# Kernel tuning notes

Hardware: AMD Instinct MI355X
Metric: run time of the kernel (lower is better)

## Reference

```python
import jax, jax.numpy as jnp
import numpy as np
from jax import lax

NUM_CLASSES = 5
K_MAX = 5
PROTO_DIM = 32
MARGIN = 1.0
ANCHOR_STRENGTH = 1.0
LAMBDA_COMPACT = 0.1
MAX_ANCHORS = 2048
KMEANS_ITERS = 5
EPS = 1e-12


def _normalize(x, axis=-1):
    return x / jnp.sqrt(jnp.sum(x * x, axis=axis, keepdims=True) + EPS)


def _cdist(a, b):
    # Euclidean distance matrix (n, m) via the squared-norm expansion.
    d2 = (jnp.sum(a * a, 1)[:, None] + jnp.sum(b * b, 1)[None, :] - 2.0 * (a @ b.T))
    return jnp.sqrt(jnp.maximum(d2, 0.0))


def _class_centroids(feats, mask, key):
    # feats: (N, D) L2-normalized; mask: (N,) bool selecting this class's voxels.
    N, D = feats.shape
    w = mask.astype(feats.dtype)
    cnt = w.sum()
    mean = (feats * w[:, None]).sum(0) / jnp.maximum(cnt, 1.0)

    def kmeans(_):
        k_init, k_fb = jax.random.split(key)
        # random init: K distinct masked points (gumbel top-k == randperm sample)
        g0 = jax.random.gumbel(k_init, (N,))
        _, init_idx = lax.top_k(jnp.where(mask, g0, -jnp.inf), K_MAX)
        cent0 = feats[init_idx]
        # fallback random masked points for empty clusters, one set per iter
        g2 = jax.random.gumbel(k_fb, (KMEANS_ITERS, N))
        fb_idx = jax.vmap(lambda s: lax.top_k(jnp.where(mask, s, -jnp.inf), K_MAX)[1])(g2)

        def body(cent, fb):
            d = _cdist(feats, cent)                       # (N, K)
            assign = jnp.argmin(d, axis=1)
            onehot = ((assign[:, None] == jnp.arange(K_MAX)[None, :]) & mask[:, None]).astype(feats.dtype)
            counts = onehot.sum(0)                        # (K,)
            sums = onehot.T @ feats                       # (K, D)
            newc = sums / jnp.maximum(counts, 1.0)[:, None]
            newc = jnp.where(counts[:, None] > 0, newc, feats[fb])
            return newc, None

        cent, _ = lax.scan(body, cent0, fb_idx)
        return _normalize(cent)

    def mean_rep(_):
        return jnp.tile(mean[None, :], (K_MAX, 1))

    cent = lax.cond(cnt >= K_MAX, kmeans, mean_rep, None)
    return _normalize(cent), cnt


def _loss_triplet(feats, prototypes, pseudo_masks, gt_masks, labeled_batch):
    B, Df, Zf, Yf, Xf = feats.shape
    N = B * Zf * Yf * Xf
    feats_flat = _normalize(jnp.transpose(feats, (0, 2, 3, 4, 1)).reshape(N, Df))
    # masks are already at feature resolution -> nearest interp is identity
    gt_flat = gt_masks.reshape(-1)
    pseudo_flat = pseudo_masks.reshape(-1)
    protos = _normalize(prototypes)                       # (C, K, D)
    key = jax.random.key(42)

    # ---- anchor loss: match prototypes to per-class kmeans centroids ----
    anchor_loss = jnp.float32(0.0)
    anchor_cnt = jnp.float32(0.0)
    for i in range(int(labeled_batch.shape[0])):
        c = labeled_batch[i]
        c_safe = jnp.clip(c, 0, NUM_CLASSES - 1)
        cmask = gt_flat == c
        cent, cnt = _class_centroids(feats_flat, cmask, jax.random.fold_in(key, i))
        valid = ((c != 0) & (c < NUM_CLASSES) & (cnt > 0)).astype(jnp.float32)
        loss_c = jnp.mean((protos[c_safe] - cent) ** 2)
        anchor_loss = anchor_loss + valid * loss_c
        anchor_cnt = anchor_cnt + valid
    anchor_loss = anchor_loss / jnp.maximum(anchor_cnt, 1.0)

    # ---- compactness: unbiased variance across the K prototypes per class ----
    compact_loss = jnp.var(protos[1:], axis=1, ddof=1).mean(axis=1).sum()

    # ---- triplet loss over pseudo-labeled anchors ----
    amask = pseudo_flat > 0
    ga = jax.random.gumbel(jax.random.fold_in(key, 1000), (N,))
    top_s, aidx = lax.top_k(jnp.where(amask, ga, -jnp.inf), MAX_ANCHORS)
    sel_valid = jnp.isfinite(top_s)                        # padding if < MAX_ANCHORS anchors
    a_feats = feats_flat[aidx]                             # (A, D)
    a_labels = jnp.clip(pseudo_flat[aidx], 0, NUM_CLASSES - 1)

    CK = NUM_CLASSES * K_MAX
    protos_flat = protos.reshape(CK, Df)
    col_cls = jnp.arange(CK) // K_MAX
    own = col_cls[None, :] == a_labels[:, None]            # (A, CK)

    sim = a_feats @ protos_flat.T
    pos_idx = jnp.argmax(jnp.where(own, sim, -jnp.inf), axis=1)
    pos_vecs = protos_flat[pos_idx]

    d_all = _cdist(a_feats, protos_flat)                   # (A, CK)
    pos_d = jnp.min(jnp.where(own, d_all, jnp.inf), axis=1)
    neg = ~own
    semi = neg & (d_all > pos_d[:, None]) & (d_all < pos_d[:, None] + MARGIN)
    g1 = jax.random.gumbel(jax.random.fold_in(key, 2000), (MAX_ANCHORS, CK))
    g2 = jax.random.gumbel(jax.random.fold_in(key, 2001), (MAX_ANCHORS, CK))
    idx_semi = jnp.argmax(jnp.where(semi, g1, -jnp.inf), axis=1)
    idx_rand = jnp.argmax(jnp.where(neg, g2, -jnp.inf), axis=1)
    neg_idx = jnp.where(semi.any(axis=1), idx_semi, idx_rand)
    neg_vecs = protos_flat[neg_idx]

    aN, pN, nN = _normalize(a_feats), _normalize(pos_vecs), _normalize(neg_vecs)
    d_pos = jnp.sqrt(jnp.sum((aN - pN) ** 2, axis=1) + EPS)
    d_neg = jnp.sqrt(jnp.sum((aN - nN) ** 2, axis=1) + EPS)
    wA = (sel_valid & (a_labels != 0)).astype(jnp.float32)
    proto_loss = jnp.sum(jax.nn.softplus(d_pos - d_neg + MARGIN) * wA) / jnp.maximum(wA.sum(), 1.0)

    return proto_loss + ANCHOR_STRENGTH * anchor_loss + LAMBDA_COMPACT * compact_loss


def setup_inputs() -> dict:
    key = jax.random.key(0)
    k1, k2, k3, k4 = jax.random.split(key, 4)
    B, Z = 4, 64
    feats = jax.random.normal(k1, (B, PROTO_DIM, Z, Z, Z), dtype=jnp.float32)
    protos = jax.random.normal(k2, (NUM_CLASSES, K_MAX, PROTO_DIM), dtype=jnp.float32)
    protos = _normalize(protos)
    pseudo_masks = jax.random.randint(k3, (B, Z, Z, Z), 0, NUM_CLASSES, dtype=jnp.int32)
    gt_masks = jax.random.randint(k4, (B, Z, Z, Z), 0, NUM_CLASSES, dtype=jnp.int32)
    labeled_batch = jnp.array([1, 2, 3, 4], dtype=jnp.int32)
    return {"feats": feats, "prototypes": protos, "pseudo_masks": pseudo_masks,
            "gt_masks": gt_masks, "labeled_batch": labeled_batch}


def reference(feats, prototypes, pseudo_masks, gt_masks, labeled_batch):
    return _loss_triplet(feats, prototypes, pseudo_masks, gt_masks, labeled_batch)
```

## Files before the change

### kernel.cpp

```cpp
#include <hip/hip_runtime.h>
#include <stdint.h>

typedef unsigned int u32;
typedef unsigned long long u64;

#define NCLS 5
#define KMX 5
#define DD 32
#define LBN 4
#define KIT 5
#define MAXA 2048
#define CKK 25
#define NBLKA 256
#define SCPAD 36
#define PSTRIDE 680
#define ACAP 8192
#define UKTHR ((1u << 23) + 1u - (1u << 15))
#define FTINY 1.17549435e-38f

struct RKeys {
  u32 ki[LBN][2];
  u32 kf[LBN][2];
  u32 k1000[2];
  u32 k2000[2];
  u32 k2001[2];
};

struct SelState {
  u32 prefix1, rank1, prefix21, rank2, pivot_sv, target, M, ncand, ncand2;
};

__host__ __device__ inline void tf2x32(u32 k0, u32 k1, u32 x0, u32 x1, u32* o0, u32* o1) {
  u32 ks2 = k0 ^ k1 ^ 0x1BD11BDAu;
  u32 ks[3] = {k0, k1, ks2};
  x0 += k0; x1 += k1;
  const int rotA[4] = {13, 15, 26, 6};
  const int rotB[4] = {17, 29, 16, 24};
#pragma unroll
  for (int g = 0; g < 5; ++g) {
#pragma unroll
    for (int j = 0; j < 4; ++j) {
      int r = (g & 1) ? rotB[j] : rotA[j];
      x0 += x1;
      x1 = (x1 << r) | (x1 >> (32 - r));
      x1 ^= x0;
    }
    x0 += ks[(g + 1) % 3];
    x1 += ks[(g + 2) % 3] + (u32)(g + 1);
  }
  *o0 = x0; *o1 = x1;
}

__device__ inline u32 jax_ukey(u32 k0, u32 k1, u32 half, u32 idx) {
  bool hi = (idx >= half);
  u32 c0 = hi ? (idx - half) : idx;
  u32 c1 = hi ? idx : (idx + half);
  u32 o0, o1;
  tf2x32(k0, k1, c0, c1, &o0, &o1);
  u32 bits = hi ? o1 : o0;
  return (bits >> 9) + 1u;
}

#define INS5(kk, a0, a1, a2, a3, a4) do { u64 _k = (kk); \
  if (_k > a4) { a4 = _k; u64 _t; \
    if (a4 > a3) { _t = a3; a3 = a4; a4 = _t; } \
    if (a3 > a2) { _t = a2; a2 = a3; a3 = _t; } \
    if (a2 > a1) { _t = a1; a1 = a2; a2 = _t; } \
    if (a1 > a0) { _t = a0; a0 = a1; a1 = _t; } } } while (0)

#define WMERGE5(off, a0, a1, a2, a3, a4) do { \
  u64 r0 = __shfl_xor(a0, off, 64), r1 = __shfl_xor(a1, off, 64), \
      r2 = __shfl_xor(a2, off, 64), r3 = __shfl_xor(a3, off, 64), \
      r4 = __shfl_xor(a4, off, 64); \
  INS5(r0, a0, a1, a2, a3, a4); INS5(r1, a0, a1, a2, a3, a4); \
  INS5(r2, a0, a1, a2, a3, a4); INS5(r3, a0, a1, a2, a3, a4); \
  INS5(r4, a0, a1, a2, a3, a4); } while (0)

#define WMERGE_ALL(a0,a1,a2,a3,a4) do { \
  WMERGE5(32,a0,a1,a2,a3,a4); WMERGE5(16,a0,a1,a2,a3,a4); WMERGE5(8,a0,a1,a2,a3,a4); \
  WMERGE5(4,a0,a1,a2,a3,a4); WMERGE5(2,a0,a1,a2,a3,a4); WMERGE5(1,a0,a1,a2,a3,a4); } while (0)

__device__ inline float rsum32(float v) {
#pragma unroll
  for (int o = 16; o; o >>= 1) v += __shfl_xor(v, o, 32);
  return v;
}

__device__ inline float rsum64(float v) {
#pragma unroll
  for (int o = 32; o; o >>= 1) v += __shfl_xor(v, o, 64);
  return v;
}


__global__ void k_protos(const float* __restrict__ protos, float* __restrict__ protn, float* __restrict__ compact) {
  __shared__ float pl[CKK * DD];
  __shared__ float rn[CKK];
  __shared__ float red[4];
  int tid = threadIdx.x;
  for (int t = tid; t < CKK * DD; t += 256) pl[t] = protos[t];
  __syncthreads();
  if (tid < CKK) {
    float s = 0.f;
    for (int d = 0; d < DD; ++d) { float x = pl[tid * DD + d]; s += x * x; }
    rn[tid] = sqrtf(s + 1e-12f);
  }
  __syncthreads();
  for (int t = tid; t < CKK * DD; t += 256) {
    float v = pl[t] / rn[t / DD];
    pl[t] = v;
    protn[t] = v;
  }
  __syncthreads();
  float part = 0.f;
  if (tid < (NCLS - 1) * DD) {
    int c = 1 + tid / DD;
    int d = tid % DD;
    float m = 0.f;
#pragma unroll
    for (int k = 0; k < KMX; ++k) m += pl[(c * KMX + k) * DD + d];
    m *= (1.0f / KMX);
    float v = 0.f;
#pragma unroll
    for (int k = 0; k < KMX; ++k) { float df = pl[(c * KMX + k) * DD + d] - m; v += df * df; }
    part = v * (1.0f / (KMX - 1)) * (1.0f / DD);
  }
#pragma unroll
  for (int o = 32; o; o >>= 1) part += __shfl_xor(part, o, 64);
  int wid = tid >> 6;
  if ((tid & 63) == 0) red[wid] = part;
  __syncthreads();
  if (tid == 0) compact[0] = red[0] + red[1] + red[2] + red[3];
}


#define T5PROC_THR(gv_, nn_) do { \
  int ci = (gv_ == lb0) ? 0 : (gv_ == lb1) ? 1 : (gv_ == lb2) ? 2 : (gv_ == lb3) ? 3 : -1; \
  if (ci >= 0) { \
    u32 k0 = (ci & 2) ? ((ci & 1) ? ka3 : ka2) : ((ci & 1) ? ka1 : ka0); \
    u32 k1 = (ci & 2) ? ((ci & 1) ? kb3 : kb2) : ((ci & 1) ? kb1 : kb0); \
    u32 uk = jax_ukey(k0, k1, half, base + (u32)(nn_)); \
    if (uk >= UKTHR) { \
      u64 key = ((u64)uk << 32) | (u32)(~(u32)(nn_)); \
      if (ci == 0) { INS5(key, A0, A1, A2, A3, A4); } \
      else if (ci == 1) { INS5(key, B0, B1, B2, B3, B4); } \
      else if (ci == 2) { INS5(key, C0, C1, C2, C3, C4); } \
      else { INS5(key, D0, D1, D2, D3, D4); } \
    } \
  } } while (0)

#define T5PROC(gv_, nn_) do { \
  int ci = (gv_ == lb0) ? 0 : (gv_ == lb1) ? 1 : (gv_ == lb2) ? 2 : (gv_ == lb3) ? 3 : -1; \
  if (ci >= 0) { \
    u32 k0 = (ci & 2) ? ((ci & 1) ? ka3 : ka2) : ((ci & 1) ? ka1 : ka0); \
    u32 k1 = (ci & 2) ? ((ci & 1) ? kb3 : kb2) : ((ci & 1) ? kb1 : kb0); \
    u32 uk = jax_ukey(k0, k1, half, base + (u32)(nn_)); \
    u64 key = ((u64)uk << 32) | (u32)(~(u32)(nn_)); \
    if (ci == 0) { INS5(key, A0, A1, A2, A3, A4); } \
    else if (ci == 1) { INS5(key, B0, B1, B2, B3, B4); } \
    else if (ci == 2) { INS5(key, C0, C1, C2, C3, C4); } \
    else { INS5(key, D0, D1, D2, D3, D4); } \
  } } while (0)

#define T5_TAIL_STORE() \
  WMERGE_ALL(A0,A1,A2,A3,A4); \
  WMERGE_ALL(B0,B1,B2,B3,B4); \
  WMERGE_ALL(C0,C1,C2,C3,C4); \
  WMERGE_ALL(D0,D1,D2,D3,D4); \
  __shared__ u64 wbuf[4][20]; \
  int tid = threadIdx.x; \
  int wid = tid >> 6; \
  if ((tid & 63) == 0) { \
    u64* w = wbuf[wid]; \
    w[0]=A0; w[1]=A1; w[2]=A2; w[3]=A3; w[4]=A4; \
    w[5]=B0; w[6]=B1; w[7]=B2; w[8]=B3; w[9]=B4; \
    w[10]=C0; w[11]=C1; w[12]=C2; w[13]=C3; w[14]=C4; \
    w[15]=D0; w[16]=D1; w[17]=D2; w[18]=D3; w[19]=D4; \
  } \
  __syncthreads(); \
  if (tid == 0) { \
    _Pragma("unroll") \
    for (int w = 1; w < 4; ++w) { \
      _Pragma("unroll") \
      for (int j = 0; j < 5; ++j) { \
        u64 ka = wbuf[w][j];      INS5(ka, A0, A1, A2, A3, A4); \
        u64 kb = wbuf[w][5 + j];  INS5(kb, B0, B1, B2, B3, B4); \
        u64 kc = wbuf[w][10 + j]; INS5(kc, C0, C1, C2, C3, C4); \
        u64 kd = wbuf[w][15 + j]; INS5(kd, D0, D1, D2, D3, D4); \
      } \
    } \
    size_t nb = gridDim.x; \
    u64* o0 = outA + (((size_t)kind * LBN + 0) * nb + blockIdx.x) * 5; \
    o0[0]=A0; o0[1]=A1; o0[2]=A2; o0[3]=A3; o0[4]=A4; \
    u64* o1 = outA + (((size_t)kind * LBN + 1) * nb + blockIdx.x) * 5; \
    o1[0]=B0; o1[1]=B1; o1[2]=B2; o1[3]=B3; o1[4]=B4; \
    u64* o2 = outA + (((size_t)kind * LBN + 2) * nb + blockIdx.x) * 5; \
    o2[0]=C0; o2[1]=C1; o2[2]=C2; o2[3]=C3; o2[4]=C4; \
    u64* o3 = outA + (((size_t)kind * LBN + 3) * nb + blockIdx.x) * 5; \
    o3[0]=D0; o3[1]=D1; o3[2]=D2; o3[3]=D3; o3[4]=D4; \
  }

#define T5_HEAD() \
  int kind = blockIdx.y; \
  int lb0 = labeled[0], lb1 = labeled[1], lb2 = labeled[2], lb3 = labeled[3]; \
  u32 half = (kind == 0) ? (u32)(N / 2) : (u32)(((u64)5 * (u64)N) / 2); \
  u32 base = (kind == 0) ? 0u : (u32)((u64)(kind - 1) * (u64)N); \
  u32 ka0 = (kind == 0) ? RK.ki[0][0] : RK.kf[0][0], kb0 = (kind == 0) ? RK.ki[0][1] : RK.kf[0][1]; \
  u32 ka1 = (kind == 0) ? RK.ki[1][0] : RK.kf[1][0], kb1 = (kind == 0) ? RK.ki[1][1] : RK.kf[1][1]; \
  u32 ka2 = (kind == 0) ? RK.ki[2][0] : RK.kf[2][0], kb2 = (kind == 0) ? RK.ki[2][1] : RK.kf[2][1]; \
  u32 ka3 = (kind == 0) ? RK.ki[3][0] : RK.kf[3][0], kb3 = (kind == 0) ? RK.ki[3][1] : RK.kf[3][1]; \
  u64 A0=0,A1=0,A2=0,A3=0,A4=0; \
  u64 B0=0,B1=0,B2=0,B3=0,B4=0; \
  u64 C0=0,C1=0,C2=0,C3=0,C4=0; \
  u64 D0=0,D1=0,D2=0,D3=0,D4=0;

__global__ void k_top5A(const int* __restrict__ gt, const int* __restrict__ labeled,
                        RKeys RK, u64* __restrict__ outA, int N) {
  T5_HEAD()
  int Nq = N >> 2;
  int stride = gridDim.x * blockDim.x;
  for (int q = blockIdx.x * blockDim.x + threadIdx.x; q < Nq; q += stride) {
    int4 g4 = ((const int4*)gt)[q];
    int n = q << 2;
    T5PROC_THR(g4.x, n);
    T5PROC_THR(g4.y, n + 1);
    T5PROC_THR(g4.z, n + 2);
    T5PROC_THR(g4.w, n + 3);
  }
  T5_TAIL_STORE()
}

__global__ void k_top5B(const u64* __restrict__ outA, u32* __restrict__ rescue,
                        u64* __restrict__ top5F, int nblk) {
  int kind = blockIdx.x;
  int i = blockIdx.y;
  const u64* src = outA + ((size_t)kind * LBN + i) * nblk * 5;
  u64 t0 = 0, t1 = 0, t2 = 0, t3 = 0, t4 = 0;
  int tot = nblk * 5;
  for (int j = threadIdx.x; j < tot; j += blockDim.x) { u64 k = src[j]; INS5(k, t0, t1, t2, t3, t4); }
  WMERGE_ALL(t0, t1, t2, t3, t4);
  __shared__ u64 wbuf[4 * 5];
  int tid = threadIdx.x;
  int wid = tid >> 6;
  if ((tid & 63) == 0) {
    wbuf[wid * 5 + 0] = t0; wbuf[wid * 5 + 1] = t1; wbuf[wid * 5 + 2] = t2;
    wbuf[wid * 5 + 3] = t3; wbuf[wid * 5 + 4] = t4;
  }
  __syncthreads();
  if (tid == 0) {
#pragma unroll
    for (int w = 1; w < 4; ++w)
#pragma unroll
      for (int j = 0; j < 5; ++j) { u64 k = wbuf[w * 5 + j]; INS5(k, t0, t1, t2, t3, t4); }
    u64* o = top5F + ((size_t)kind * LBN + i) * 5;
    o[0] = t0; o[1] = t1; o[2] = t2; o[3] = t3; o[4] = t4;
    if (t4 == 0ULL) atomicOr(rescue, 1u << (kind * 4 + i));
  }
}

__global__ void k_top5A_resc(const int* __restrict__ gt, const int* __restrict__ labeled,
                             RKeys RK, const u32* __restrict__ rescue,
                             u64* __restrict__ outA, int N) {
  if (((rescue[0] >> (blockIdx.y * 4)) & 0xFu) == 0u) return;
  T5_HEAD()
  int Nq = N >> 2;
  int stride = gridDim.x * blockDim.x;
  for (int q = blockIdx.x * blockDim.x + threadIdx.x; q < Nq; q += stride) {
    int4 g4 = ((const int4*)gt)[q];
    int n = q << 2;
    T5PROC(g4.x, n);
    T5PROC(g4.y, n + 1);
    T5PROC(g4.z, n + 2);
    T5PROC(g4.w, n + 3);
  }
  T5_TAIL_STORE()
}

__global__ void k_top5B_resc(const u64* __restrict__ outA, const u32* __restrict__ rescue,
                             u64* __restrict__ top5F, int nblk) {
  int kind = blockIdx.x;
  int i = blockIdx.y;
  if (!((rescue[0] >> (kind * 4 + i)) & 1u)) return;
  const u64* src = outA + ((size_t)kind * LBN + i) * nblk * 5;
  u64 t0 = 0, t1 = 0, t2 = 0, t3 = 0, t4 = 0;
  int tot = nblk * 5;
  for (int j = threadIdx.x; j < tot; j += blockDim.x) { u64 k = src[j]; INS5(k, t0, t1, t2, t3, t4); }
  WMERGE_ALL(t0, t1, t2, t3, t4);
  __shared__ u64 wbuf[4 * 5];
  int tid = threadIdx.x;
  int wid = tid >> 6;
  if ((tid & 63) == 0) {
    wbuf[wid * 5 + 0] = t0; wbuf[wid * 5 + 1] = t1; wbuf[wid * 5 + 2] = t2;
    wbuf[wid * 5 + 3] = t3; wbuf[wid * 5 + 4] = t4;
  }
  __syncthreads();
  if (tid == 0) {
#pragma unroll
    for (int w = 1; w < 4; ++w)
#pragma unroll
      for (int j = 0; j < 5; ++j) { u64 k = wbuf[w * 5 + j]; INS5(k, t0, t1, t2, t3, t4); }
    u64* o = top5F + ((size_t)kind * LBN + i) * 5;
    o[0] = t0; o[1] = t1; o[2] = t2; o[3] = t3; o[4] = t4;
  }
}


__global__ void __launch_bounds__(256)
k_normT(const float* __restrict__ feats, float4* __restrict__ featsN4, int N, int Z3) {
  __shared__ float xl[256 * 33];
  __shared__ float sinv[256];
  int tid = threadIdx.x;
  int nchunk = N >> 8;
  for (int chunk = blockIdx.x; chunk < nchunk; chunk += gridDim.x) {
    int n0 = chunk << 8;
    int b = n0 / Z3, v0 = n0 - b * Z3;
    const float* fp = feats + (size_t)b * DD * Z3 + v0 + tid;
#pragma unroll
    for (int d = 0; d < DD; ++d) xl[tid * 33 + d] = fp[(size_t)d * Z3];
    float s = 0.f;
#pragma unroll
    for (int d = 0; d < DD; ++d) { float x = xl[tid * 33 + d]; s += x * x; }
    sinv[tid] = 1.0f / sqrtf(s + 1e-12f);
    __syncthreads();
#pragma unroll
    for (int i = 0; i < 8; ++i) {
      int fi = i * 256 + tid;
      int vox = fi >> 3, q = fi & 7;
      float iv = sinv[vox];
      float4 o;
      o.x = xl[vox * 33 + q * 4 + 0] * iv;
      o.y = xl[vox * 33 + q * 4 + 1] * iv;
      o.z = xl[vox * 33 + q * 4 + 2] * iv;
      o.w = xl[vox * 33 + q * 4 + 3] * iv;
      featsN4[(size_t)n0 * 8 + fi] = o;
    }
    __syncthreads();
  }
}

__global__ void k_initcentT(const float* __restrict__ featsN,
                            const u64* __restrict__ top5F, float* __restrict__ cent, int N) {
  int t = threadIdx.x;
  if (t >= LBN * KMX * DD) return;
  int d = t & 31;
  int k = (t >> 5) % KMX;
  int i = t / (KMX * DD);
  u32 n = ~(u32)(top5F[((size_t)0 * LBN + i) * 5 + k]);
  if (n >= (u32)N) n = 0;
  cent[(i * KMX + k) * DD + d] = featsN[(size_t)n * DD + d];
}

__global__ void __launch_bounds__(256)
k_assignW2(const float4* __restrict__ featsN4, const int* __restrict__ gt,
           const int* __restrict__ labeled, const float* __restrict__ cent,
           float* __restrict__ part, int N) {
  __shared__ float sc[LBN * KMX * SCPAD];
  __shared__ float ssw[8][LBN * KMX * SCPAD];
  __shared__ float scn[LBN * KMX];
  __shared__ float scw[8][LBN * KMX];
  int tid = threadIdx.x;
  for (int t = tid; t < LBN * KMX * DD; t += 256) {
    int cl2 = t >> 5, d = t & 31;
    sc[cl2 * SCPAD + d] = cent[t];
  }
  for (int t = tid; t < 8 * LBN * KMX * SCPAD; t += 256) (&ssw[0][0])[t] = 0.f;
  for (int t = tid; t < 8 * LBN * KMX; t += 256) (&scw[0][0])[t] = 0.f;
  __syncthreads();
  if (tid < LBN * KMX) {
    float s = 0.f;
#pragma unroll
    for (int d = 0; d < DD; ++d) { float c = sc[tid * SCPAD + d]; s += c * c; }
    scn[tid] = s;
  }
  __syncthreads();
  int lb0 = labeled[0], lb1 = labeled[1], lb2 = labeled[2], lb3 = labeled[3];
  int q = tid & 7;
  int grp = (tid >> 3) & 7;
  int wv = tid >> 6;
  int cpi = 2 * wv + (grp >> 2);
  float* myss = &ssw[cpi][0];
  float* mysc = &scw[cpi][0];
  int sstep = grp & 3;
  const float* scq = sc + q * 4;
  int nchunk = N >> 5;
  int chunk = blockIdx.x;
  if (chunk < nchunk) {
    float4 f4 = featsN4[(size_t)chunk * 256 + tid];
    int g = gt[(chunk << 5) + (tid >> 3)];
    while (true) {
      int nxt = chunk + gridDim.x;
      bool has = nxt < nchunk;
      float4 nf4; int ng = 0;
      if (has) {
        nf4 = featsN4[(size_t)nxt * 256 + tid];
        ng = gt[(nxt << 5) + (tid >> 3)];
      }
      int ci = (g == lb0) ? 0 : (g == lb1) ? 1 : (g == lb2) ? 2 : (g == lb3) ? 3 : -1;
      int basec = (ci < 0 ? 0 : ci) * KMX;
      float4 c0 = *(const float4*)(scq + (basec + 0) * SCPAD);
      float4 c1 = *(const float4*)(scq + (basec + 1) * SCPAD);
      float4 c2 = *(const float4*)(scq + (basec + 2) * SCPAD);
      float4 c3 = *(const float4*)(scq + (basec + 3) * SCPAD);
      float4 c4 = *(const float4*)(scq + (basec + 4) * SCPAD);
      float p0 = f4.x * c0.x + f4.y * c0.y + f4.z * c0.z + f4.w * c0.w;
      float p1 = f4.x * c1.x + f4.y * c1.y + f4.z * c1.z + f4.w * c1.w;
      float p2 = f4.x * c2.x + f4.y * c2.y + f4.z * c2.z + f4.w * c2.w;
      float p3 = f4.x * c3.x + f4.y * c3.y + f4.z * c3.z + f4.w * c3.w;
      float p4 = f4.x * c4.x + f4.y * c4.y + f4.z * c4.z + f4.w * c4.w;
#pragma unroll
      for (int o = 1; o < 8; o <<= 1) {
        p0 += __shfl_xor(p0, o, 64);
        p1 += __shfl_xor(p1, o, 64);
        p2 += __shfl_xor(p2, o, 64);
        p3 += __shfl_xor(p3, o, 64);
        p4 += __shfl_xor(p4, o, 64);
      }
      float bd = scn[basec + 0] - 2.0f * p0; int bk = 0;
      float d2;
      d2 = scn[basec + 1] - 2.0f * p1; if (d2 < bd) { bd = d2; bk = 1; }
      d2 = scn[basec + 2] - 2.0f * p2; if (d2 < bd) { bd = d2; bk = 2; }
      d2 = scn[basec + 3] - 2.0f * p3; if (d2 < bd) { bd = d2; bk = 3; }
      d2 = scn[basec + 4] - 2.0f * p4; if (d2 < bd) { bd = d2; bk = 4; }
      int cl = basec + bk;
#pragma unroll
      for (int s = 0; s < 4; ++s) {
        if (sstep == s && ci >= 0) {
          float* dst = myss + cl * SCPAD + q * 4;
          float4 cur = *(float4*)dst;
          cur.x += f4.x; cur.y += f4.y; cur.z += f4.z; cur.w += f4.w;
          *(float4*)dst = cur;
          if (q == 0) mysc[cl] += 1.0f;
        }
      }
      if (!has) break;
      chunk = nxt; f4 = nf4; g = ng;
    }
  }
  __syncthreads();
  float* po = part + (size_t)blockIdx.x * PSTRIDE;
  for (int p = tid; p < 660; p += 256) {
    float v;
    if (p < 640) {
      int idx = (p >> 5) * SCPAD + (p & 31);
      v = ssw[0][idx] + ssw[1][idx] + ssw[2][idx] + ssw[3][idx]
        + ssw[4][idx] + ssw[5][idx] + ssw[6][idx] + ssw[7][idx];
    } else {
      int ik = p - 640;
      v = scw[0][ik] + scw[1][ik] + scw[2][ik] + scw[3][ik]
        + scw[4][ik] + scw[5][ik] + scw[6][ik] + scw[7][ik];
    }
    po[p] = v;
  }
}

__global__ void k_redupdT(const float* __restrict__ part, const float* __restrict__ featsN,
                          const u64* __restrict__ top5F, float* __restrict__ cent,
                          float* __restrict__ sums, float* __restrict__ kcnt,
                          int iter, int N, int NB) {
  __shared__ float w4[8];
  int p = blockIdx.x;
  int tid = threadIdx.x;
  if (p < 640) {
    int ik = p >> 5, d = p & 31;
    float s = 0.f, c = 0.f;
    for (int b2 = tid; b2 < NB; b2 += 256) {
      s += part[(size_t)b2 * PSTRIDE + p];
      c += part[(size_t)b2 * PSTRIDE + 640 + ik];
    }
    s = rsum64(s); c = rsum64(c);
    int wid = tid >> 6;
    if ((tid & 63) == 0) { w4[wid] = s; w4[4 + wid] = c; }
    __syncthreads();
    if (tid == 0) {
      float S = w4[0] + w4[1] + w4[2] + w4[3];
      float C = w4[4] + w4[5] + w4[6] + w4[7];
      sums[p] = S;
      if (C > 0.f) {
        cent[p] = S / fmaxf(C, 1.0f);
      } else {
        int i = ik / KMX, k = ik % KMX;
        u32 n = ~(u32)(top5F[((size_t)(1 + iter) * LBN + i) * 5 + k]);
        if (n >= (u32)N) n = 0;
        cent[p] = featsN[(size_t)n * DD + d];
      }
    }
  } else if (p < 660) {
    int ik = p - 640;
    float c = 0.f;
    for (int b2 = tid; b2 < NB; b2 += 256) c += part[(size_t)b2 * PSTRIDE + 640 + ik];
    c = rsum64(c);
    int wid = tid >> 6;
    if ((tid & 63) == 0) w4[wid] = c;
    __syncthreads();
    if (tid == 0) kcnt[ik] = w4[0] + w4[1] + w4[2] + w4[3];
  }
}

__global__ void k_prepT(const float4* __restrict__ featsN4,
                        const int* __restrict__ pseudo, const SelState* __restrict__ st,
                        const int* __restrict__ aidx, float4* __restrict__ afe4,
                        int* __restrict__ alab, int N) {
  int tid = threadIdx.x;
  int r = blockIdx.x * 32 + (tid >> 3);
  int q = tid & 7;
  if (r >= (int)st->target) return;
  int n = aidx[r];
  if ((u32)n >= (u32)N) n = 0;
  if (q == 0) {
    int lb = pseudo[n];
    alab[r] = lb < 0 ? 0 : (lb > NCLS - 1 ? NCLS - 1 : lb);
  }
  afe4[(size_t)r * 8 + q] = featsN4[(size_t)n * 8 + q];
}


__global__ void __launch_bounds__(256)
k_anchsel(const int* __restrict__ pseudo, RKeys RK, u64* __restrict__ cand8k,
          SelState* st, int N) {
  __shared__ u32 mcnt[4];
  u32 K0 = RK.k1000[0], K1 = RK.k1000[1];
  u32 half = (u32)(N / 2);
  int tid = threadIdx.x;
  int lcnt = 0;
  int stride = gridDim.x * blockDim.x;
  for (int n = blockIdx.x * blockDim.x + tid; n < N; n += stride) {
    bool valid = pseudo[n] > 0;
    lcnt += valid ? 1 : 0;
    u32 uk = jax_ukey(K0, K1, half, (u32)n);
    bool c = valid && (uk >= UKTHR);
    if (__ballot(c)) {
      if (c) {
        u32 p = atomicAdd(&st->ncand, 1u);
        if (p < (u32)ACAP) cand8k[p] = ((u64)uk << 32) | (u32)(~(u32)n);
      }
    }
  }
#pragma unroll
  for (int o = 32; o; o >>= 1) lcnt += __shfl_xor(lcnt, o, 64);
  if ((tid & 63) == 0) mcnt[tid >> 6] = (u32)lcnt;
  __syncthreads();
  if (tid == 0) atomicAdd(&st->M, mcnt[0] + mcnt[1] + mcnt[2] + mcnt[3]);
}

__global__ void k_selmode(SelState* st, u32* rescue) {
  if (threadIdx.x != 0 || blockIdx.x != 0) return;
  u32 M = st->M;
  u32 tgt = M < (u32)MAXA ? M : (u32)MAXA;
  st->target = tgt;
  if (!(st->ncand >= tgt && st->ncand <= (u32)ACAP)) rescue[1] = 1u;
}

__global__ void __launch_bounds__(1024)
k_sortsel8k(const u64* __restrict__ cand8k, const SelState* __restrict__ st,
            const u32* __restrict__ rescue, int* __restrict__ aidx) {
  if (rescue[1]) return;
  __shared__ u64 s[ACAP];
  u32 nc = st->ncand; if (nc > (u32)ACAP) nc = (u32)ACAP;
  u32 target = st->target;
  for (int t = threadIdx.x; t < ACAP; t += blockDim.x) s[t] = (t < (int)nc) ? cand8k[t] : 0ULL;
  __syncthreads();
  for (u32 ksz = 2; ksz <= (u32)ACAP; ksz <<= 1) {
    for (u32 j = ksz >> 1; j > 0; j >>= 1) {
      for (u32 idx = threadIdx.x; idx < (u32)ACAP; idx += blockDim.x) {
        u32 ixj = idx ^ j;
        if (ixj > idx) {
          bool up = (idx & ksz) == 0;
          u64 A = s[idx], B = s[ixj];
          bool sw = up ? (A < B) : (A > B);
          if (sw) { s[idx] = B; s[ixj] = A; }
        }
      }
      __syncthreads();
    }
  }
  for (int t = threadIdx.x; t < MAXA; t += blockDim.x)
    if (t < (int)target) aidx[t] = (int)(~(u32)s[t]);
}


__global__ void k_svinit(const int* __restrict__ pseudo, RKeys RK, const u32* __restrict__ rescue,
                         u32* __restrict__ sv, u32* __restrict__ hist, int N) {
  if (!rescue[1]) return;
  __shared__ u32 h[2048];
  for (int t = threadIdx.x; t < 2048; t += blockDim.x) h[t] = 0;
  __syncthreads();
  u32 half = (u32)(N / 2);
  u32 K0 = RK.k1000[0], K1 = RK.k1000[1];
  int Nq = N >> 2;
  int stride = gridDim.x * blockDim.x;
  for (int q = blockIdx.x * blockDim.x + threadIdx.x; q < Nq; q += stride) {
    int4 p4 = ((const int4*)pseudo)[q];
    int n = q << 2;
    u32 s0 = 0, s1 = 0, s2 = 0, s3 = 0;
    if (p4.x > 0) { s0 = jax_ukey(K0, K1, half, (u32)n);     atomicAdd(&h[s0 >> 21], 1u); }
    if (p4.y > 0) { s1 = jax_ukey(K0, K1, half, (u32)n + 1); atomicAdd(&h[s1 >> 21], 1u); }
    if (p4.z > 0) { s2 = jax_ukey(K0, K1, half, (u32)n + 2); atomicAdd(&h[s2 >> 21], 1u); }
    if (p4.w > 0) { s3 = jax_ukey(K0, K1, half, (u32)n + 3); atomicAdd(&h[s3 >> 21], 1u); }
    ((uint4*)sv)[q] = make_uint4(s0, s1, s2, s3);
  }
  __syncthreads();
  for (int t = threadIdx.x; t < 2048; t += blockDim.x) if (h[t]) atomicAdd(&hist[t], h[t]);
}

__global__ void k_hist12(const u32* __restrict__ sv, u32* __restrict__ hist,
                         const SelState* __restrict__ st, const u32* __restrict__ rescue,
                         int pass, int N) {
  if (!rescue[1]) return;
  __shared__ u32 h[2048];
  for (int t = threadIdx.x; t < 2048; t += blockDim.x) h[t] = 0;
  __syncthreads();
  u32 pre = (pass == 1) ? st->prefix1 : st->prefix21;
  int Nq = N >> 2;
  int stride = gridDim.x * blockDim.x;
  for (int q = blockIdx.x * blockDim.x + threadIdx.x; q < Nq; q += stride) {
    uint4 s4 = ((const uint4*)sv)[q];
#define H12(s_) do { u32 s = (s_); if (s) { \
      if (pass == 1) { if ((s >> 21) == pre) atomicAdd(&h[(s >> 10) & 0x7FFu], 1u); } \
      else           { if ((s >> 10) == pre) atomicAdd(&h[s & 0x3FFu], 1u); } } } while (0)
    H12(s4.x); H12(s4.y); H12(s4.z); H12(s4.w);
#undef H12
  }
  __syncthreads();
  for (int t = threadIdx.x; t < 2048; t += blockDim.x) if (h[t]) atomicAdd(&hist[t], h[t]);
}

__global__ void k_scan(const u32* __restrict__ hist, SelState* st,
                       const u32* __restrict__ rescue, int pass) {
  if (!rescue[1]) return;
  __shared__ u32 h[2048];
  __shared__ u32 csum[256];
  __shared__ u32 sh_rank;
  __shared__ int sh_found;
  __shared__ u32 sh_rem;
  int tid = threadIdx.x;
  int nb = (pass == 2) ? 1024 : 2048;
  for (int t = tid; t < 2048; t += 256) h[t] = (t < nb) ? hist[t] : 0u;
  __syncthreads();
  u32 cs = 0;
#pragma unroll
  for (int j = 0; j < 8; ++j) cs += h[tid * 8 + j];
  csum[tid] = cs;
  __syncthreads();
  if (tid == 0) {
    sh_rank = (pass == 0) ? st->target : (pass == 1 ? st->rank1 : st->rank2);
    sh_found = -1;
    sh_rem = 0;
  }
  __syncthreads();
  u32 rank = sh_rank;
  if (rank > 0) {
    u32 above = 0;
    for (int j = tid + 1; j < 256; ++j) above += csum[j];
    u32 run = above;
    for (int b = tid * 8 + 7; b >= tid * 8; --b) {
      u32 c = h[b];
      if (run < rank && rank <= run + c) { sh_found = b; sh_rem = rank - run; }
      run += c;
    }
  }
  __syncthreads();
  if (tid == 0) {
    int found = sh_found;
    u32 rem = sh_rem;
    if (pass == 0) {
      if (found < 0) { st->prefix1 = 0xFFFFFFFFu; st->rank1 = 0; }
      else { st->prefix1 = (u32)found; st->rank1 = rem; }
    } else if (pass == 1) {
      if (found < 0) { st->prefix21 = 0xFFFFFFFFu; st->rank2 = 0; }
      else { st->prefix21 = (st->prefix1 << 11) | (u32)found; st->rank2 = rem; }
    } else {
      if (found < 0) st->pivot_sv = 0xFFFFFFFFu;
      else st->pivot_sv = (st->prefix21 << 10) | (u32)found;
    }
  }
}

__global__ void k_gather(const u32* __restrict__ sv, SelState* st,
                         const u32* __restrict__ rescue, u64* __restrict__ cand, int N) {
  if (!rescue[1]) return;
  if (st->target == 0) return;
  u32 piv = st->pivot_sv;
  int Nq = N >> 2;
  int stride = gridDim.x * blockDim.x;
  for (int q = blockIdx.x * blockDim.x + threadIdx.x; q < Nq; q += stride) {
    uint4 s4 = ((const uint4*)sv)[q];
    int n = q << 2;
#define GPUSH(s_, nn_) do { u32 s = (s_); \
    if (s && s >= piv) { u32 p = atomicAdd(&st->ncand2, 1u); \
      if (p < 4096u) cand[p] = ((u64)s << 32) | (u32)(~(u32)(nn_)); } } while (0)
    GPUSH(s4.x, n); GPUSH(s4.y, n + 1); GPUSH(s4.z, n + 2); GPUSH(s4.w, n + 3);
#undef GPUSH
  }
}

__global__ void __launch_bounds__(1024) k_sortsel(const u64* __restrict__ cand,
                                                  const SelState* __restrict__ st,
                                                  const u32* __restrict__ rescue,
                                                  int* __restrict__ aidx) {
  if (!rescue[1]) return;
  __shared__ u64 s[4096];
  u32 nc = st->ncand2; if (nc > 4096u) nc = 4096u;
  u32 target = st->target;
  for (int t = threadIdx.x; t < 4096; t += blockDim.x) s[t] = (t < (int)nc) ? cand[t] : 0ULL;
  __syncthreads();
  for (u32 ksz = 2; ksz <= 4096; ksz <<= 1) {
    for (u32 j = ksz >> 1; j > 0; j >>= 1) {
      for (u32 idx = threadIdx.x; idx < 4096; idx += blockDim.x) {
        u32 ixj = idx ^ j;
        if (ixj > idx) {
          bool up = (idx & ksz) == 0;
          u64 A = s[idx], B = s[ixj];
          bool sw = up ? (A < B) : (A > B);
          if (sw) { s[idx] = B; s[ixj] = A; }
        }
      }
      __syncthreads();
    }
  }
  for (int t = threadIdx.x; t < MAXA; t += blockDim.x)
    if (t < (int)target) aidx[t] = (int)(~(u32)s[t]);
}


__global__ void k_anchor_final(const float* __restrict__ cent, const float* __restrict__ sums,
                               const float* __restrict__ kcnt, const float* __restrict__ protn,
                               const int* __restrict__ labeled, float* __restrict__ accum) {
  int i = blockIdx.x;
  int d = threadIdx.x;
  if (d >= DD) return;
  int c = labeled[i];
  float cnt = 0.f;
#pragma unroll
  for (int k = 0; k < KMX; ++k) cnt += kcnt[i * KMX + k];
  int cs = c < 0 ? 0 : (c > NCLS - 1 ? NCLS - 1 : c);
  float part = 0.f;
  if (cnt >= (float)KMX) {
#pragma unroll
    for (int k = 0; k < KMX; ++k) {
      float v = cent[(i * KMX + k) * DD + d];
      float s = rsum32(v * v);
      float dn1 = sqrtf(s + 1e-12f);
      float v1 = v / dn1;
      float s2 = rsum32(v1 * v1);
      float dn2 = sqrtf(s2 + 1e-12f);
      float vv = v1 / dn2;
      float df = protn[(cs * KMX + k) * DD + d] - vv;
      part += df * df;
    }
  } else {
    float mv = 0.f;
#pragma unroll
    for (int k = 0; k < KMX; ++k) mv += sums[(i * KMX + k) * DD + d];
    mv /= fmaxf(cnt, 1.0f);
    float s = rsum32(mv * mv);
    float dn = sqrtf(s + 1e-12f);
    float vv = mv / dn;
#pragma unroll
    for (int k = 0; k < KMX; ++k) {
      float df = protn[(cs * KMX + k) * DD + d] - vv;
      part += df * df;
    }
  }
  float ls = rsum32(part) * (1.0f / (KMX * DD));
  bool valid = (c != 0) && (c < NCLS) && (cnt > 0.f);
  if (d == 0 && valid) { atomicAdd(&accum[0], ls); atomicAdd(&accum[1], 1.0f); }
}

__global__ void k_triplet(const float* __restrict__ protn, const float* __restrict__ afe,
                          const int* __restrict__ alab, const SelState* __restrict__ st,
                          RKeys RK, float* __restrict__ acc) {
  __shared__ float pn[CKK * DD];
  __shared__ float spn[CKK];
  int tid = threadIdx.x;
  for (int t = tid; t < CKK * DD; t += blockDim.x) pn[t] = protn[t];
  __syncthreads();
  if (tid < CKK) {
    float s = 0.f;
    for (int d = 0; d < DD; ++d) s += pn[tid * DD + d] * pn[tid * DD + d];
    spn[tid] = s;
  }
  __syncthreads();
  int r = blockIdx.x * blockDim.x + tid;
  if (r >= (int)st->target) return;
  float a[DD]; float sa = 0.f;
#pragma unroll
  for (int d = 0; d < DD; ++d) { a[d] = afe[(size_t)r * DD + d]; sa += a[d] * a[d]; }
  int lab = alab[r];
  int ob = lab * KMX;
  float bs = -3.4e38f; int pidx = ob;
  float pos_d = 3.4e38f;
  for (int k = ob; k < ob + KMX; ++k) {
    float dot = 0.f;
#pragma unroll
    for (int d = 0; d < DD; ++d) dot += a[d] * pn[k * DD + d];
    if (dot > bs) { bs = dot; pidx = k; }
    float d2 = (sa + spn[k]) - 2.0f * dot;
    float dd = sqrtf(fmaxf(d2, 0.f));
    pos_d = fminf(pos_d, dd);
  }
  u32 halfT = (u32)(MAXA * CKK / 2);
  bool any_semi = false;
  u32 bu1 = 0; int k1i = 0;
  u32 bu2 = 0; int k2i = 0;
  for (int k = 0; k < CKK; ++k) {
    if (k / KMX == lab) continue;
    float dot = 0.f;
#pragma unroll
    for (int d = 0; d < DD; ++d) dot += a[d] * pn[k * DD + d];
    float d2 = (sa + spn[k]) - 2.0f * dot;
    float dd = sqrtf(fmaxf(d2, 0.f));
    u32 j = (u32)(r * CKK + k);
    bool semi = (dd > pos_d) && (dd < pos_d + 1.0f);
    if (semi) {
      u32 u1 = jax_ukey(RK.k2000[0], RK.k2000[1], halfT, j);
      any_semi = true;
      if (u1 > bu1) { bu1 = u1; k1i = k; }
    }
    u32 u2 = jax_ukey(RK.k2001[0], RK.k2001[1], halfT, j);
    if (u2 > bu2) { bu2 = u2; k2i = k; }
  }
  int nidx = any_semi ? k1i : k2i;
  float aden = sqrtf(sa + 1e-12f);
  float pden = sqrtf(spn[pidx] + 1e-12f);
  float nden = sqrtf(spn[nidx] + 1e-12f);
  float s1 = 0.f, s2 = 0.f;
#pragma unroll
  for (int d = 0; d < DD; ++d) {
    float an = a[d] / aden;
    float pv = pn[pidx * DD + d] / pden;
    float nv = pn[nidx * DD + d] / nden;
    float t1 = an - pv; s1 += t1 * t1;
    float t2 = an - nv; s2 += t2 * t2;
  }
  float d_pos = sqrtf(s1 + 1e-12f);
  float d_neg = sqrtf(s2 + 1e-12f);
  float xx = (d_pos - d_neg) + 1.0f;
  float l = fmaxf(xx, 0.f) + log1pf(expf(-fabsf(xx)));
  atomicAdd(&acc[0], l);
  atomicAdd(&acc[1], 1.0f);
}

__global__ void k_final(const float* __restrict__ anchor_acc, const float* __restrict__ proto_acc,
                        const float* __restrict__ compact, float* __restrict__ out) {
  if (threadIdx.x != 0 || blockIdx.x != 0) return;
  float al = anchor_acc[0] / fmaxf(anchor_acc[1], 1.0f);
  float pl = proto_acc[0] / fmaxf(proto_acc[1], 1.0f);
  out[0] = pl + 1.0f * al + 0.1f * compact[0];
}


static void host_keys(RKeys* K) {
  const u32 b0 = 0u, b1 = 42u;
  u32 o0, o1;
  for (int i = 0; i < LBN; ++i) {
    u32 f0, f1;
    tf2x32(b0, b1, 0u, (u32)i, &f0, &f1);
    u32 p0, q0, p1, q1;
    tf2x32(f0, f1, 0u, 2u, &p0, &q0);
    tf2x32(f0, f1, 1u, 3u, &p1, &q1);
    K->ki[i][0] = p0; K->ki[i][1] = p1;
    K->kf[i][0] = q0; K->kf[i][1] = q1;
  }
  tf2x32(b0, b1, 0u, 1000u, &o0, &o1); K->k1000[0] = o0; K->k1000[1] = o1;
  tf2x32(b0, b1, 0u, 2000u, &o0, &o1); K->k2000[0] = o0; K->k2000[1] = o1;
  tf2x32(b0, b1, 0u, 2001u, &o0, &o1); K->k2001[0] = o0; K->k2001[1] = o1;
}

extern "C" void kernel_launch(void* const* d_in, const int* in_sizes, int n_in,
                              void* d_out, int out_size, void* d_ws, size_t ws_size,
                              hipStream_t stream) {
  const float* feats = (const float*)d_in[0];
  const float* protos = (const float*)d_in[1];
  const int* pseudo = (const int*)d_in[2];
  const int* gt = (const int*)d_in[3];
  const int* labeled = (const int*)d_in[4];
  float* out = (float*)d_out;

  int N = in_sizes[2];
  int Z3 = N / 4;

  RKeys RK;
  host_keys(&RK);

  const int nbas[3] = {1280, 640, 320};
  for (int attempt = 0; attempt < 3; ++attempt) {
    int NBAS = nbas[attempt];
    char* W = (char*)d_ws;
    size_t off = 0;
    auto alloc = [&](size_t bytes) -> char* {
      char* p = W + off;
      off += (bytes + 255) & ~(size_t)255;
      return p;
    };
    char* zeroBase = W + off;
    u32* hist3 = (u32*)alloc(3 * 2048 * 4);
    SelState* st = (SelState*)alloc(256);
    float* anchor_acc = (float*)alloc(256);
    float* proto_acc = (float*)alloc(256);
    u32* rescue = (u32*)alloc(256);
    size_t zeroBytes = (size_t)((W + off) - zeroBase);
    u64* cand8k = (u64*)alloc((size_t)ACAP * 8);
    u64* outA = (u64*)alloc((size_t)6 * LBN * NBLKA * 5 * 8);
    u64* top5F = (u64*)alloc((size_t)6 * LBN * 5 * 8);
    float* cent = (float*)alloc((size_t)LBN * KMX * DD * 4);
    float* sums = (float*)alloc((size_t)LBN * KMX * DD * 4);
    float* kcnt = (float*)alloc((size_t)LBN * KMX * 4);
    float* protn = (float*)alloc((size_t)CKK * DD * 4);
    float* compact = (float*)alloc(256);
    u32* sv = (u32*)alloc((size_t)N * 4);
    float* part = (float*)alloc((size_t)NBAS * PSTRIDE * 4);
    u64* cand = (u64*)alloc(4096 * 8);
    int* aidx = (int*)alloc((size_t)MAXA * 4);
    int* alab = (int*)alloc((size_t)MAXA * 4);
    float* afe = (float*)alloc((size_t)MAXA * DD * 4);
    float* featsN = (float*)alloc((size_t)N * DD * 4);
    if (ws_size < off) continue;

    hipMemsetAsync(zeroBase, 0, zeroBytes, stream);

    k_protos<<<dim3(1), dim3(256), 0, stream>>>(protos, protn, compact);

    k_top5A<<<dim3(NBLKA, 6), dim3(256), 0, stream>>>(gt, labeled, RK, outA, N);
    k_top5B<<<dim3(6, LBN), dim3(256), 0, stream>>>(outA, rescue, top5F, NBLKA);
    k_top5A_resc<<<dim3(NBLKA, 6), dim3(256), 0, stream>>>(gt, labeled, RK, rescue, outA, N);
    k_top5B_resc<<<dim3(6, LBN), dim3(256), 0, stream>>>(outA, rescue, top5F, NBLKA);

    float4* featsN4 = (float4*)featsN;
    k_normT<<<dim3(2048), dim3(256), 0, stream>>>(feats, featsN4, N, Z3);
    k_initcentT<<<dim3(1), dim3(LBN * KMX * DD), 0, stream>>>(featsN, top5F, cent, N);
    for (int it = 0; it < KIT; ++it) {
      k_assignW2<<<dim3(NBAS), dim3(256), 0, stream>>>(featsN4, gt, labeled, cent, part, N);
      k_redupdT<<<dim3(660), dim3(256), 0, stream>>>(part, featsN, top5F, cent, sums, kcnt, it, N, NBAS);
    }
    k_anchor_final<<<dim3(LBN), dim3(64), 0, stream>>>(cent, sums, kcnt, protn, labeled, anchor_acc);

    k_anchsel<<<dim3(2048), dim3(256), 0, stream>>>(pseudo, RK, cand8k, st, N);
    k_selmode<<<dim3(1), dim3(64), 0, stream>>>(st, rescue);
    k_svinit<<<dim3(1024), dim3(256), 0, stream>>>(pseudo, RK, rescue, sv, hist3, N);
    k_scan<<<dim3(1), dim3(256), 0, stream>>>(hist3, st, rescue, 0);
    k_hist12<<<dim3(1024), dim3(256), 0, stream>>>(sv, hist3 + 2048, st, rescue, 1, N);
    k_scan<<<dim3(1), dim3(256), 0, stream>>>(hist3 + 2048, st, rescue, 1);
    k_hist12<<<dim3(1024), dim3(256), 0, stream>>>(sv, hist3 + 4096, st, rescue, 2, N);
    k_scan<<<dim3(1), dim3(256), 0, stream>>>(hist3 + 4096, st, rescue, 2);
    k_gather<<<dim3(1024), dim3(256), 0, stream>>>(sv, st, rescue, cand, N);
    k_sortsel<<<dim3(1), dim3(1024), 0, stream>>>(cand, st, rescue, aidx);
    k_sortsel8k<<<dim3(1), dim3(1024), 0, stream>>>(cand8k, st, rescue, aidx);

    k_prepT<<<dim3(MAXA / 32), dim3(256), 0, stream>>>(featsN4, pseudo, st, aidx,
                                                        (float4*)afe, alab, N);
    k_triplet<<<dim3(MAXA / 256), dim3(256), 0, stream>>>(protn, afe, alab, st, RK, proto_acc);

    k_final<<<dim3(1), dim3(64), 0, stream>>>(anchor_acc, proto_acc, compact, out);
    return;
  }
}
```

Measured before the change: 681.1 us.

## Replace single-block bitonic sort with multi-block rank-by-counting selection

The single-workgroup 8192-element bitonic sort of anchor candidates is replaced by a rank computation spread across 16 blocks: each thread counts how many candidate keys exceed its own and writes its index to that rank slot if it falls under the target. The candidate capacity is halved to 4096, which shrinks shared memory and the O(n^2) counting work. The cost is that fewer candidate sets fit in the fast path, so more inputs may fall back to the slower histogram-based rescue path. Each block also reloads every key into LDS.

Result: faster. 614.3 us (-9.8%).

```diff
diff --git a/kernel.cpp b/kernel.cpp
--- a/kernel.cpp
+++ b/kernel.cpp
@@ -14,7 +14,7 @@
 #define NBLKA 256
 #define SCPAD 36
 #define PSTRIDE 680
-#define ACAP 8192
+#define ACAP 4096
 #define UKTHR ((1u << 23) + 1u - (1u << 15))
 #define FTINY 1.17549435e-38f
 
@@ -515,7 +515,7 @@
 
 
 __global__ void __launch_bounds__(256)
-k_anchsel(const int* __restrict__ pseudo, RKeys RK, u64* __restrict__ cand8k,
+k_anchsel(const int* __restrict__ pseudo, RKeys RK, u64* __restrict__ cand4k,
           SelState* st, int N) {
   __shared__ u32 mcnt[4];
   u32 K0 = RK.k1000[0], K1 = RK.k1000[1];
@@ -531,7 +531,7 @@
     if (__ballot(c)) {
       if (c) {
         u32 p = atomicAdd(&st->ncand, 1u);
-        if (p < (u32)ACAP) cand8k[p] = ((u64)uk << 32) | (u32)(~(u32)n);
+        if (p < (u32)ACAP) cand4k[p] = ((u64)uk << 32) | (u32)(~(u32)n);
       }
     }
   }
@@ -550,31 +550,22 @@
   if (!(st->ncand >= tgt && st->ncand <= (u32)ACAP)) rescue[1] = 1u;
 }
 
-__global__ void __launch_bounds__(1024)
-k_sortsel8k(const u64* __restrict__ cand8k, const SelState* __restrict__ st,
-            const u32* __restrict__ rescue, int* __restrict__ aidx) {
+__global__ void __launch_bounds__(256)
+k_rank(const u64* __restrict__ cand4k, const SelState* __restrict__ st,
+       const u32* __restrict__ rescue, int* __restrict__ aidx) {
   if (rescue[1]) return;
-  __shared__ u64 s[ACAP];
+  __shared__ u64 keys[ACAP];
   u32 nc = st->ncand; if (nc > (u32)ACAP) nc = (u32)ACAP;
   u32 target = st->target;
-  for (int t = threadIdx.x; t < ACAP; t += blockDim.x) s[t] = (t < (int)nc) ? cand8k[t] : 0ULL;
-  __syncthreads();
-  for (u32 ksz = 2; ksz <= (u32)ACAP; ksz <<= 1) {
-    for (u32 j = ksz >> 1; j > 0; j >>= 1) {
-      for (u32 idx = threadIdx.x; idx < (u32)ACAP; idx += blockDim.x) {
-        u32 ixj = idx ^ j;
-        if (ixj > idx) {
-          bool up = (idx & ksz) == 0;
-          u64 A = s[idx], B = s[ixj];
-          bool sw = up ? (A < B) : (A > B);
-          if (sw) { s[idx] = B; s[ixj] = A; }
-        }
-      }
-      __syncthreads();
-    }
-  }
-  for (int t = threadIdx.x; t < MAXA; t += blockDim.x)
-    if (t < (int)target) aidx[t] = (int)(~(u32)s[t]);
+  int tid = threadIdx.x;
+  for (int t = tid; t < ACAP; t += 256) keys[t] = (t < (int)nc) ? cand4k[t] : 0ULL;
+  __syncthreads();
+  int i = blockIdx.x * 256 + tid;
+  if (i >= (int)nc) return;
+  u64 my = keys[i];
+  u32 rank = 0;
+  for (u32 j = 0; j < nc; ++j) rank += (keys[j] > my) ? 1u : 0u;
+  if (rank < target) aidx[rank] = (int)(~(u32)my);
 }
 
 
@@ -899,7 +890,7 @@
     float* proto_acc = (float*)alloc(256);
     u32* rescue = (u32*)alloc(256);
     size_t zeroBytes = (size_t)((W + off) - zeroBase);
-    u64* cand8k = (u64*)alloc((size_t)ACAP * 8);
+    u64* cand4k = (u64*)alloc((size_t)ACAP * 8);
     u64* outA = (u64*)alloc((size_t)6 * LBN * NBLKA * 5 * 8);
     u64* top5F = (u64*)alloc((size_t)6 * LBN * 5 * 8);
     float* cent = (float*)alloc((size_t)LBN * KMX * DD * 4);
@@ -934,7 +925,7 @@
     }
     k_anchor_final<<<dim3(LBN), dim3(64), 0, stream>>>(cent, sums, kcnt, protn, labeled, anchor_acc);
 
-    k_anchsel<<<dim3(2048), dim3(256), 0, stream>>>(pseudo, RK, cand8k, st, N);
+    k_anchsel<<<dim3(2048), dim3(256), 0, stream>>>(pseudo, RK, cand4k, st, N);
     k_selmode<<<dim3(1), dim3(64), 0, stream>>>(st, rescue);
     k_svinit<<<dim3(1024), dim3(256), 0, stream>>>(pseudo, RK, rescue, sv, hist3, N);
     k_scan<<<dim3(1), dim3(256), 0, stream>>>(hist3, st, rescue, 0);
@@ -944,7 +935,7 @@
     k_scan<<<dim3(1), dim3(256), 0, stream>>>(hist3 + 4096, st, rescue, 2);
     k_gather<<<dim3(1024), dim3(256), 0, stream>>>(sv, st, rescue, cand, N);
     k_sortsel<<<dim3(1), dim3(1024), 0, stream>>>(cand, st, rescue, aidx);
-    k_sortsel8k<<<dim3(1), dim3(1024), 0, stream>>>(cand8k, st, rescue, aidx);
+    k_rank<<<dim3(ACAP / 256), dim3(256), 0, stream>>>(cand4k, st, rescue, aidx);
 
     k_prepT<<<dim3(MAXA / 32), dim3(256), 0, stream>>>(featsN4, pseudo, st, aidx,
                                                         (float4*)afe, alab, N);
```
